# Kernel tuning notes

Measured on AMD Instinct MI355X. Metric: run time of the kernel, lower is better.

Reference implementation:

```python
import jax, jax.numpy as jnp
import numpy as np
from jax import lax

B, N = 8, 4096
NPOINT, RADIUS, NSAMPLE = 1024, 0.2, 32
MLP = [64, 64, 128]
FEAT = 64
ALPHA = 0.2          # LeakyReLU slope
BN_EPS = 1e-5        # BatchNorm eps (eval mode, running_mean=0, running_var=1)
BIG = 1e10


def setup_inputs() -> dict:
    key = jax.random.key(0)
    ks = jax.random.split(key, 16)
    xyz = jax.random.uniform(ks[0], (B, N, 3), dtype=jnp.float32)
    feats = jax.random.normal(ks[1], (B, N, FEAT), dtype=jnp.float32)
    d = {"points": jnp.concatenate([xyz, feats], axis=-1)}
    ch = [FEAT] + MLP
    for i in range(len(MLP)):
        d[f"W{i}"] = jax.random.normal(ks[2 + 3 * i], (ch[i + 1], ch[i]), dtype=jnp.float32) * 0.1
        d[f"b{i}"] = jnp.zeros((ch[i + 1],), jnp.float32)
        d[f"g{i}"] = jnp.ones((ch[i + 1],), jnp.float32)
        d[f"be{i}"] = jnp.zeros((ch[i + 1],), jnp.float32)
    d["a_att"] = jax.random.uniform(ks[12], (3 + MLP[-1], MLP[-1]), jnp.float32, -0.3, 0.3)
    return d


def _gather(points, idx):
    # points: [B, N, D], idx: [B, ...] -> [B, ..., D]
    return jax.vmap(lambda p, i: p[i])(points, idx)


def farthest_point_sample(xyz, npoint):
    # xyz: [B, N, 3] -> [B, npoint] (deterministic start at index 0)
    b, n, _ = xyz.shape
    def step(carry, _):
        distance, farthest = carry
        centered = jnp.take_along_axis(xyz, farthest[:, None, None], axis=1)  # [B,1,3]
        dist = jnp.sum((xyz - centered) ** 2, axis=-1)                        # [B,N]
        distance = jnp.minimum(distance, dist)
        return (distance, jnp.argmax(distance, axis=-1)), farthest
    init = (jnp.full((b, n), BIG, dtype=xyz.dtype), jnp.zeros((b,), dtype=jnp.int32))
    _, idxs = lax.scan(step, init, None, length=npoint)
    return jnp.transpose(idxs)  # [B, npoint]


def query_ball_point(nsample, radius, xyz, centered_xyz):
    # squared distances [B, npoint, N]
    d = (-2.0 * jnp.einsum('bpc,bnc->bpn', centered_xyz, xyz)
         + jnp.sum(centered_xyz ** 2, -1)[..., None]
         + jnp.sum(xyz ** 2, -1)[:, None, :])
    d = jnp.where(d > radius ** 2, BIG, d)
    order = jnp.argsort(d, axis=-1)[..., :nsample]                    # [B,np,ns]
    sv = jnp.take_along_axis(d, order, axis=-1)                       # sorted values
    first = order[..., 0:1]
    return jnp.where(sv == BIG, first, order)


def _mlp(x, params):
    # x: [..., C]; 1x1 conv + BN(eval, mean=0, var=1) + relu per layer
    for (W, b, g, be) in params:
        x = jnp.einsum('...c,oc->...o', x, W) + b
        x = x * (g / jnp.sqrt(1.0 + BN_EPS)) + be
        x = jax.nn.relu(x)
    return x


def reference(points, W0, b0, g0, be0, W1, b1, g1, be1, W2, b2, g2, be2, a_att):
    xyz = points[..., :3]
    feats = points[..., 3:]
    cidx = farthest_point_sample(xyz, NPOINT)          # [B, npoint]
    cxyz = _gather(xyz, cidx)                          # [B, npoint, 3]
    cfeat = _gather(feats, cidx)                       # [B, npoint, D]
    gidx = query_ball_point(NSAMPLE, RADIUS, xyz, cxyz)  # [B, npoint, nsample]
    gxyz = _gather(xyz, gidx)                          # [B, npoint, ns, 3]
    gfeat = _gather(feats, gidx)                       # [B, npoint, ns, D]

    params = [(W0, b0, g0, be0), (W1, b1, g1, be1), (W2, b2, g2, be2)]
    cfeat = _mlp(cfeat, params)                        # [B, npoint, D']
    gfeat = _mlp(gfeat, params)                        # [B, npoint, ns, D']

    cpts = jnp.concatenate([cxyz, cfeat], axis=-1)     # [B, npoint, 3+D']
    gpts = jnp.concatenate([gxyz, gfeat], axis=-1)     # [B, npoint, ns, 3+D']

    delta = gpts - cpts[:, :, None, :]
    att = jax.nn.leaky_relu(jnp.einsum('bpnc,cd->bpnd', delta, a_att), ALPHA)
    att = jax.nn.softmax(att, axis=2)                  # over nsample (eval: no dropout)
    gac = jnp.sum(att * gfeat, axis=2)                 # [B, npoint, D']
    return jnp.concatenate([cxyz, gac], axis=-1)       # [B, npoint, 3+D']
```

## Files before the change

### kernel.cpp

```cpp
#include <hip/hip_runtime.h>
#include <math.h>

#define NBATCH 8
#define NPTS 4096
#define NPOINT 1024
#define NSAMPLE 32
#define PTDIM 67
#define BIGF 1e10f

#define DPP_QUAD_XOR1 0xB1
#define DPP_QUAD_XOR2 0x4E
#define DPP_ROW_HALF_MIRROR 0x141
#define DPP_ROW_MIRROR 0x140
#define DPP_ROW_BCAST15 0x142
#define DPP_ROW_BCAST31 0x143

template <int CTRL>
__device__ inline float dpp_mov_f(float v) {
  int i = __float_as_int(v);
  return __int_as_float(__builtin_amdgcn_update_dpp(i, i, CTRL, 0xf, 0xf, false));
}
template <int CTRL>
__device__ inline unsigned dpp_mov_u(unsigned v) {
  return (unsigned)__builtin_amdgcn_update_dpp((int)v, (int)v, CTRL, 0xf, 0xf, false);
}
template <int CTRL>
__device__ inline void dpp_min2(unsigned& hi, unsigned& lo) {
  unsigned nh = dpp_mov_u<CTRL>(hi);
  unsigned nl = dpp_mov_u<CTRL>(lo);
  bool take = (nh < hi) || (nh == hi && nl < lo);
  hi = take ? nh : hi;
  lo = take ? nl : lo;
}
__device__ inline unsigned fmap(float d) {
  unsigned b = __float_as_uint(d);
  return ((int)b < 0) ? ~b : (b | 0x80000000u);
}
#define FMAP_INF 0xFF800000u

__device__ inline float red32_max(float v) {
  v = fmaxf(v, dpp_mov_f<DPP_QUAD_XOR1>(v));
  v = fmaxf(v, dpp_mov_f<DPP_QUAD_XOR2>(v));
  v = fmaxf(v, dpp_mov_f<DPP_ROW_HALF_MIRROR>(v));
  v = fmaxf(v, dpp_mov_f<DPP_ROW_MIRROR>(v));
  v = fmaxf(v, __shfl_xor(v, 16));
  return v;
}
__device__ inline float red32_sum(float v) {
  v += dpp_mov_f<DPP_QUAD_XOR1>(v);
  v += dpp_mov_f<DPP_QUAD_XOR2>(v);
  v += dpp_mov_f<DPP_ROW_HALF_MIRROR>(v);
  v += dpp_mov_f<DPP_ROW_MIRROR>(v);
  v += __shfl_xor(v, 16);
  return v;
}

struct FpsS {
  unsigned long long slots[2][4];
  int cidxS[NPOINT];
  float4 C[NPTS];
};
struct ProjS {
  float As[131 * 128];
  float w0[64 * 64], w1[64 * 64], w2[128 * 64];
  float bb0[64], ss0[64], ee0[64];
  float bb1[64], ss1[64], ee1[64];
  float bb2[128], ss2[128], ee2[128];
};
#define F1_SMEM (sizeof(ProjS) > sizeof(FpsS) ? sizeof(ProjS) : sizeof(FpsS))

__device__ void fps_body(char* smemRaw, const float* __restrict__ pts,
                         int* __restrict__ cidx, float* __restrict__ X,
                         float* __restrict__ Y, float* __restrict__ Z) {
#pragma clang fp contract(off)
  FpsS* S = (FpsS*)smemRaw;
  const int b = blockIdx.x, tid = threadIdx.x;
  const int w = tid >> 6, lane = tid & 63;
  const float* pb = pts + (size_t)b * NPTS * PTDIM;
  float2 px2[8], py2[8], pz2[8];
  float dl[16];
  #pragma unroll
  for (int k = 0; k < 16; k++) {
    int j = tid + (k << 8);
    const float* pj = pb + (size_t)j * PTDIM;
    float x = pj[0], y = pj[1], z = pj[2];
    if (k & 1) { px2[k >> 1].y = x; py2[k >> 1].y = y; pz2[k >> 1].y = z; }
    else       { px2[k >> 1].x = x; py2[k >> 1].x = y; pz2[k >> 1].x = z; }
    S->C[j] = make_float4(x, y, z, 0.0f);
    X[b * NPTS + j] = x; Y[b * NPTS + j] = y; Z[b * NPTS + j] = z;
    dl[k] = BIGF;
  }
  __syncthreads();
  int f = 0;
  float4 c0 = S->C[0];
  float cx = c0.x, cy = c0.y, cz = c0.z;
  for (int t = 0; t < NPOINT; t++) {
    if (tid == 0) S->cidxS[t] = f;
    float2 c2x = make_float2(cx, cx);
    float2 c2y = make_float2(cy, cy);
    float2 c2z = make_float2(cz, cz);
    #pragma unroll
    for (int m = 0; m < 8; m++) {
      float2 dx = px2[m] - c2x;
      float2 dy = py2[m] - c2y;
      float2 dz = pz2[m] - c2z;
      float2 d = (dx * dx + dy * dy) + dz * dz;
      dl[2 * m]     = fminf(dl[2 * m],     d.x);
      dl[2 * m + 1] = fminf(dl[2 * m + 1], d.y);
    }
    float u0 = fmaxf(dl[0], dl[1]),  u1 = fmaxf(dl[2], dl[3]);
    float u2 = fmaxf(dl[4], dl[5]),  u3 = fmaxf(dl[6], dl[7]);
    float u4 = fmaxf(dl[8], dl[9]),  u5 = fmaxf(dl[10], dl[11]);
    float u6 = fmaxf(dl[12], dl[13]), u7 = fmaxf(dl[14], dl[15]);
    float v0 = fmaxf(u0, u1), v1 = fmaxf(u2, u3);
    float v2 = fmaxf(u4, u5), v3 = fmaxf(u6, u7);
    float bv = fmaxf(fmaxf(v0, v1), fmaxf(v2, v3));
    float m = bv;
    m = fmaxf(m, dpp_mov_f<DPP_QUAD_XOR1>(m));
    m = fmaxf(m, dpp_mov_f<DPP_QUAD_XOR2>(m));
    m = fmaxf(m, dpp_mov_f<DPP_ROW_HALF_MIRROR>(m));
    m = fmaxf(m, dpp_mov_f<DPP_ROW_MIRROR>(m));
    m = fmaxf(m, dpp_mov_f<DPP_ROW_BCAST15>(m));
    m = fmaxf(m, dpp_mov_f<DPP_ROW_BCAST31>(m));
    unsigned wmaxbits = (unsigned)__builtin_amdgcn_readlane(__float_as_int(m), 63);
    unsigned c_[16];
    #pragma unroll
    for (int k = 0; k < 16; k++)
      c_[k] = (__float_as_uint(dl[k]) == wmaxbits) ? (unsigned)(tid + (k << 8)) : 0xFFFFFFFFu;
    unsigned q0 = min(c_[0], c_[1]),  q1 = min(c_[2], c_[3]);
    unsigned q2 = min(c_[4], c_[5]),  q3 = min(c_[6], c_[7]);
    unsigned q4 = min(c_[8], c_[9]),  q5 = min(c_[10], c_[11]);
    unsigned q6 = min(c_[12], c_[13]), q7 = min(c_[14], c_[15]);
    unsigned r0 = min(q0, q1), r1 = min(q2, q3), r2 = min(q4, q5), r3 = min(q6, q7);
    unsigned cand = min(min(r0, r1), min(r2, r3));
    cand = min(cand, dpp_mov_u<DPP_QUAD_XOR1>(cand));
    cand = min(cand, dpp_mov_u<DPP_QUAD_XOR2>(cand));
    cand = min(cand, dpp_mov_u<DPP_ROW_HALF_MIRROR>(cand));
    cand = min(cand, dpp_mov_u<DPP_ROW_MIRROR>(cand));
    cand = min(cand, dpp_mov_u<DPP_ROW_BCAST15>(cand));
    cand = min(cand, dpp_mov_u<DPP_ROW_BCAST31>(cand));
    unsigned jmin = (unsigned)__builtin_amdgcn_readlane((int)cand, 63);
    if (lane == 0)
      S->slots[t & 1][w] = ((unsigned long long)wmaxbits << 32) |
                           (unsigned long long)(NPTS - 1 - jmin);
    __syncthreads();
    unsigned long long s0 = S->slots[t & 1][0], s1 = S->slots[t & 1][1];
    unsigned long long s2 = S->slots[t & 1][2], s3 = S->slots[t & 1][3];
    unsigned long long m0 = s0 > s1 ? s0 : s1;
    unsigned long long m1 = s2 > s3 ? s2 : s3;
    unsigned long long best = m0 > m1 ? m0 : m1;
    f = NPTS - 1 - (int)(best & 0xFFFFFFFFull);
    float4 cc = S->C[f];
    cx = cc.x; cy = cc.y; cz = cc.z;
  }
  __syncthreads();
  for (int i = tid; i < NPOINT; i += 256) cidx[b * NPOINT + i] = S->cidxS[i];
}

__device__ void projmlp_body(char* smemRaw, const float* __restrict__ pts,
    const float* __restrict__ W0, const float* __restrict__ B0, const float* __restrict__ G0, const float* __restrict__ E0,
    const float* __restrict__ W1, const float* __restrict__ B1, const float* __restrict__ G1, const float* __restrict__ E1,
    const float* __restrict__ W2, const float* __restrict__ B2, const float* __restrict__ G2, const float* __restrict__ E2,
    const float* __restrict__ Aatt,
    float* __restrict__ mfeat, float* __restrict__ P) {
  ProjS* S = (ProjS*)smemRaw;
  const float INVS = 0.99999500003750f;
  const int t = threadIdx.x;
  for (int i = t; i < 131 * 128; i += 256) S->As[i] = Aatt[i];
  for (int i = t; i < 4096; i += 256) { S->w0[i] = W0[i]; S->w1[i] = W1[i]; }
  for (int i = t; i < 8192; i += 256) S->w2[i] = W2[i];
  if (t < 64) {
    S->bb0[t] = B0[t]; S->ss0[t] = G0[t] * INVS; S->ee0[t] = E0[t];
    S->bb1[t] = B1[t]; S->ss1[t] = G1[t] * INVS; S->ee1[t] = E1[t];
  }
  if (t < 128) { S->bb2[t] = B2[t]; S->ss2[t] = G2[t] * INVS; S->ee2[t] = E2[t]; }
  __syncthreads();

  const int pb = blockIdx.x - 8;
  for (int rr = 0; rr < 2; rr++) {
    const size_t r = (size_t)pb * 512 + rr * 256 + t;
    const float* xr = pts + r * PTDIM + 3;
    float x[64];
    #pragma unroll
    for (int c = 0; c < 64; c++) x[c] = xr[c];

    float h1[64];
    #pragma unroll
    for (int o = 0; o < 64; o++) {
      float acc = S->bb0[o];
      #pragma unroll
      for (int c = 0; c < 64; c += 4) {
        float4 wv = *(const float4*)&S->w0[o * 64 + c];
        acc = fmaf(wv.x, x[c], acc);
        acc = fmaf(wv.y, x[c + 1], acc);
        acc = fmaf(wv.z, x[c + 2], acc);
        acc = fmaf(wv.w, x[c + 3], acc);
      }
      h1[o] = fmaxf(fmaf(acc, S->ss0[o], S->ee0[o]), 0.0f);
    }
    float h2[64];
    #pragma unroll
    for (int o = 0; o < 64; o++) {
      float acc = S->bb1[o];
      #pragma unroll
      for (int c = 0; c < 64; c += 4) {
        float4 wv = *(const float4*)&S->w1[o * 64 + c];
        acc = fmaf(wv.x, h1[c], acc);
        acc = fmaf(wv.y, h1[c + 1], acc);
        acc = fmaf(wv.z, h1[c + 2], acc);
        acc = fmaf(wv.w, h1[c + 3], acc);
      }
      h2[o] = fmaxf(fmaf(acc, S->ss1[o], S->ee1[o]), 0.0f);
    }
    float h3[128];
    float* orow = mfeat + r * 128;
    #pragma unroll
    for (int o = 0; o < 128; o += 4) {
      float a0 = S->bb2[o], a1 = S->bb2[o + 1], a2 = S->bb2[o + 2], a3 = S->bb2[o + 3];
      #pragma unroll
      for (int c = 0; c < 64; c += 4) {
        float4 wv0 = *(const float4*)&S->w2[(o    ) * 64 + c];
        float4 wv1 = *(const float4*)&S->w2[(o + 1) * 64 + c];
        float4 wv2 = *(const float4*)&S->w2[(o + 2) * 64 + c];
        float4 wv3 = *(const float4*)&S->w2[(o + 3) * 64 + c];
        a0 = fmaf(wv0.x, h2[c], a0); a0 = fmaf(wv0.y, h2[c+1], a0); a0 = fmaf(wv0.z, h2[c+2], a0); a0 = fmaf(wv0.w, h2[c+3], a0);
        a1 = fmaf(wv1.x, h2[c], a1); a1 = fmaf(wv1.y, h2[c+1], a1); a1 = fmaf(wv1.z, h2[c+2], a1); a1 = fmaf(wv1.w, h2[c+3], a1);
        a2 = fmaf(wv2.x, h2[c], a2); a2 = fmaf(wv2.y, h2[c+1], a2); a2 = fmaf(wv2.z, h2[c+2], a2); a2 = fmaf(wv2.w, h2[c+3], a2);
        a3 = fmaf(wv3.x, h2[c], a3); a3 = fmaf(wv3.y, h2[c+1], a3); a3 = fmaf(wv3.z, h2[c+2], a3); a3 = fmaf(wv3.w, h2[c+3], a3);
      }
      float4 ov;
      ov.x = fmaxf(fmaf(a0, S->ss2[o    ], S->ee2[o    ]), 0.0f);
      ov.y = fmaxf(fmaf(a1, S->ss2[o + 1], S->ee2[o + 1]), 0.0f);
      ov.z = fmaxf(fmaf(a2, S->ss2[o + 2], S->ee2[o + 2]), 0.0f);
      ov.w = fmaxf(fmaf(a3, S->ss2[o + 3], S->ee2[o + 3]), 0.0f);
      h3[o] = ov.x; h3[o + 1] = ov.y; h3[o + 2] = ov.z; h3[o + 3] = ov.w;
      *(float4*)(orow + o) = ov;
    }
    const float* pr = pts + r * PTDIM;
    float x0 = pr[0], y0 = pr[1], z0 = pr[2];
    float* prow = P + r * 128;
    for (int grp = 0; grp < 4; grp++) {
      const int g0 = grp * 32;
      float acc[32];
      #pragma unroll
      for (int j = 0; j < 32; j++) {
        float a0 = S->As[0 * 128 + g0 + j];
        float a1 = S->As[1 * 128 + g0 + j];
        float a2 = S->As[2 * 128 + g0 + j];
        acc[j] = fmaf(z0, a2, fmaf(y0, a1, x0 * a0));
      }
      #pragma unroll
      for (int c = 0; c < 128; c++) {
        float s = h3[c];
        const float* arow = &S->As[(3 + c) * 128 + g0];
        #pragma unroll
        for (int j = 0; j < 32; j += 4) {
          float4 a = *(const float4*)&arow[j];
          acc[j]   = fmaf(s, a.x, acc[j]);
          acc[j+1] = fmaf(s, a.y, acc[j+1]);
          acc[j+2] = fmaf(s, a.z, acc[j+2]);
          acc[j+3] = fmaf(s, a.w, acc[j+3]);
        }
      }
      #pragma unroll
      for (int j = 0; j < 32; j += 4)
        *(float4*)(prow + g0 + j) = make_float4(acc[j], acc[j+1], acc[j+2], acc[j+3]);
    }
  }
}

__global__ __launch_bounds__(256) void f1_kernel(const float* __restrict__ pts,
    const float* __restrict__ W0, const float* __restrict__ B0, const float* __restrict__ G0, const float* __restrict__ E0,
    const float* __restrict__ W1, const float* __restrict__ B1, const float* __restrict__ G1, const float* __restrict__ E1,
    const float* __restrict__ W2, const float* __restrict__ B2, const float* __restrict__ G2, const float* __restrict__ E2,
    const float* __restrict__ Aatt,
    float* __restrict__ mfeat, float* __restrict__ P, int* __restrict__ cidx,
    float* __restrict__ X, float* __restrict__ Y, float* __restrict__ Z) {
  __shared__ __align__(16) char smem[F1_SMEM];
  if (blockIdx.x < 8)
    fps_body(smem, pts, cidx, X, Y, Z);
  else
    projmlp_body(smem, pts, W0, B0, G0, E0, W1, B1, G1, E1, W2, B2, G2, E2,
                 Aatt, mfeat, P);
}

__global__ __launch_bounds__(256) void f2_kernel(
    const float* __restrict__ X, const float* __restrict__ Y, const float* __restrict__ Z,
    const int* __restrict__ cidx, int* __restrict__ gidx) {
  __shared__ float dbuf[4][512];
  __shared__ int   ibuf[4][512];
  const int t = threadIdx.x;
  const int w = t >> 6, lane = t & 63;
  const int pc = blockIdx.x * 4 + w;
  const int b = pc >> 10;
  const float* Xb = X + b * NPTS;
  const float* Yb = Y + b * NPTS;
  const float* Zb = Z + b * NPTS;
  const int cI = cidx[pc];
  const float cx = Xb[cI], cy = Yb[cI], cz = Zb[cI];
  const float sc = __fadd_rn(__fadd_rn(__fmul_rn(cx, cx), __fmul_rn(cy, cy)), __fmul_rn(cz, cz));
  const float R2 = 0.04f;
  int cnt = 0;
  for (int rr = 0; rr < 16; rr++) {
    const int base = rr * 256 + lane * 4;
    float4 px4 = *(const float4*)(Xb + base);
    float4 py4 = *(const float4*)(Yb + base);
    float4 pz4 = *(const float4*)(Zb + base);
    #pragma unroll
    for (int e = 0; e < 4; e++) {
      float px = e == 0 ? px4.x : e == 1 ? px4.y : e == 2 ? px4.z : px4.w;
      float py = e == 0 ? py4.x : e == 1 ? py4.y : e == 2 ? py4.z : py4.w;
      float pz = e == 0 ? pz4.x : e == 1 ? pz4.y : e == 2 ? pz4.z : pz4.w;
      float dot = __fadd_rn(__fadd_rn(__fmul_rn(cx, px), __fmul_rn(cy, py)), __fmul_rn(cz, pz));
      float sx  = __fadd_rn(__fadd_rn(__fmul_rn(px, px), __fmul_rn(py, py)), __fmul_rn(pz, pz));
      float d   = __fadd_rn(__fadd_rn(__fmul_rn(-2.0f, dot), sc), sx);
      bool pred = !(d > R2);
      unsigned long long mask = __ballot(pred);
      if (pred) {
        int pos = cnt + (int)__popcll(mask & ((1ull << lane) - 1ull));
        if (pos < 512) { dbuf[w][pos] = d; ibuf[w][pos] = base + e; }
      }
      cnt += (int)__popcll(mask);
    }
  }
  const int K = cnt < 512 ? cnt : 512;
  unsigned long long kk[8];
  #pragma unroll
  for (int k = 0; k < 8; k++) {
    int pos = lane + 64 * k;
    if (pos < K)
      kk[k] = ((unsigned long long)fmap(dbuf[w][pos]) << 32) | (unsigned)ibuf[w][pos];
    else
      kk[k] = ((unsigned long long)FMAP_INF << 32) | 0x7fffffffu;
  }
  int first = 0;
  int* gout = gidx + pc * NSAMPLE;
  for (int it = 0; it < NSAMPLE; it++) {
    unsigned long long best = kk[0];
    #pragma unroll
    for (int k = 1; k < 8; k++) if (kk[k] < best) best = kk[k];
    unsigned hi = (unsigned)(best >> 32), lo = (unsigned)best;
    dpp_min2<DPP_QUAD_XOR1>(hi, lo);
    dpp_min2<DPP_QUAD_XOR2>(hi, lo);
    dpp_min2<DPP_ROW_HALF_MIRROR>(hi, lo);
    dpp_min2<DPP_ROW_MIRROR>(hi, lo);
    dpp_min2<DPP_ROW_BCAST15>(hi, lo);
    dpp_min2<DPP_ROW_BCAST31>(hi, lo);
    unsigned blo = (unsigned)__builtin_amdgcn_readlane((int)lo, 63);
    #pragma unroll
    for (int k = 0; k < 8; k++)
      if ((unsigned)kk[k] == blo)
        kk[k] = (kk[k] & 0xFFFFFFFFull) | ((unsigned long long)FMAP_INF << 32);
    if (it == 0) first = (int)blo;
    if (lane == 0) gout[it] = (it < K) ? (int)blo : first;
  }
}

__global__ __launch_bounds__(256) void attn_kernel(
    const float* __restrict__ X, const float* __restrict__ Y, const float* __restrict__ Z,
    const float* __restrict__ mfeat, const float* __restrict__ P,
    const int* __restrict__ cidx, const int* __restrict__ gidx,
    float* __restrict__ out) {
  __shared__ float pcS[128];
  const int pc = (blockIdx.x & 7) * 1024 + (blockIdx.x >> 3);
  const int b = pc >> 10;
  const int t = threadIdx.x;
  const int n = t & 31, q = t >> 5;
  const int cI = cidx[pc];
  if (t < 128) pcS[t] = P[((size_t)b * NPTS + cI) * 128 + t];
  const int g = gidx[pc * NSAMPLE + n];
  const float* Pg = P + ((size_t)b * NPTS + g) * 128 + q * 16;
  const float* Gf = mfeat + ((size_t)b * NPTS + g) * 128 + q * 16;
  __syncthreads();
  float a[16], gfv[16];
  #pragma unroll
  for (int k = 0; k < 4; k++) {
    float4 vg = *(const float4*)(Pg + 4 * k);
    float4 vc = *(const float4*)&pcS[q * 16 + 4 * k];
    float4 vf = *(const float4*)(Gf + 4 * k);
    a[4*k]   = vg.x - vc.x; a[4*k+1] = vg.y - vc.y;
    a[4*k+2] = vg.z - vc.z; a[4*k+3] = vg.w - vc.w;
    gfv[4*k] = vf.x; gfv[4*k+1] = vf.y; gfv[4*k+2] = vf.z; gfv[4*k+3] = vf.w;
  }
  #pragma unroll
  for (int j = 0; j < 16; j++) a[j] = a[j] >= 0.0f ? a[j] : 0.2f * a[j];
  float e[16], s[16], num[16];
  #pragma unroll
  for (int j = 0; j < 16; j++) {
    float mx = red32_max(a[j]);
    e[j] = expf(a[j] - mx);
  }
  #pragma unroll
  for (int j = 0; j < 16; j++) s[j] = red32_sum(e[j]);
  #pragma unroll
  for (int j = 0; j < 16; j++) num[j] = red32_sum(e[j] * gfv[j]);
  if (n == 0) {
    float* orow = out + (size_t)pc * 131;
    #pragma unroll
    for (int j = 0; j < 16; j++) orow[3 + q * 16 + j] = num[j] / s[j];
    if (q == 0) {
      orow[0] = X[b * NPTS + cI]; orow[1] = Y[b * NPTS + cI]; orow[2] = Z[b * NPTS + cI];
    }
  }
}

extern "C" void kernel_launch(void* const* d_in, const int* in_sizes, int n_in,
                              void* d_out, int out_size, void* d_ws, size_t ws_size,
                              hipStream_t stream) {
  const float* points = (const float*)d_in[0];
  const float* W0 = (const float*)d_in[1];
  const float* B0 = (const float*)d_in[2];
  const float* G0 = (const float*)d_in[3];
  const float* E0 = (const float*)d_in[4];
  const float* W1 = (const float*)d_in[5];
  const float* B1 = (const float*)d_in[6];
  const float* G1 = (const float*)d_in[7];
  const float* E1 = (const float*)d_in[8];
  const float* W2 = (const float*)d_in[9];
  const float* B2 = (const float*)d_in[10];
  const float* G2 = (const float*)d_in[11];
  const float* E2 = (const float*)d_in[12];
  const float* Aatt = (const float*)d_in[13];
  float* out = (float*)d_out;

  float* mfeat = (float*)d_ws;
  float* Pw = mfeat + (size_t)NBATCH * NPTS * 128;
  float* Xw = Pw + (size_t)NBATCH * NPTS * 128;
  float* Yw = Xw + NBATCH * NPTS;
  float* Zw = Yw + NBATCH * NPTS;
  int* cidxw = (int*)(Zw + NBATCH * NPTS);
  int* gidxw = cidxw + NBATCH * NPOINT;

  f1_kernel<<<8 + 64, 256, 0, stream>>>(points,
      W0, B0, G0, E0, W1, B1, G1, E1, W2, B2, G2, E2, Aatt,
      mfeat, Pw, cidxw, Xw, Yw, Zw);
  f2_kernel<<<NBATCH * NPOINT / 4, 256, 0, stream>>>(Xw, Yw, Zw, cidxw, gidxw);
  attn_kernel<<<NBATCH * NPOINT, 256, 0, stream>>>(Xw, Yw, Zw, mfeat, Pw, cidxw, gidxw, out);
}
```

Measured before the change: 833.5 us.

## Fuse ball query with attention and forward FPS winner coordinates through slots

The ball-query kernel and the attention kernel are merged, so each block computes neighbour indices for four centroids into shared memory and then runs the softmax aggregation on them. This removes the gidx round trip through global memory and one kernel launch. In FPS, each wave now writes its candidate's coordinates next to its key in the slot, so the winner's coordinates are picked by selects instead of a dependent shared-memory load after the barrier. The cost is larger shared slots and a serial four-centroid attention loop per block, which lowers the number of parallel blocks in the attention phase.

```diff
diff --git a/kernel.cpp b/kernel.cpp
--- a/kernel.cpp
+++ b/kernel.cpp
@@ -38,6 +38,10 @@
 }
 #define FMAP_INF 0xFF800000u
 
+__device__ inline float4 sel4(bool c, float4 a, float4 b) {
+  return make_float4(c ? a.x : b.x, c ? a.y : b.y, c ? a.z : b.z, c ? a.w : b.w);
+}
+
 __device__ inline float red32_max(float v) {
   v = fmaxf(v, dpp_mov_f<DPP_QUAD_XOR1>(v));
   v = fmaxf(v, dpp_mov_f<DPP_QUAD_XOR2>(v));
@@ -55,8 +59,9 @@
   return v;
 }
 
+struct __align__(16) Slot { float4 c; unsigned long long key; unsigned long long pad; };
 struct FpsS {
-  unsigned long long slots[2][4];
+  Slot slots[2][4];
   int cidxS[NPOINT];
   float4 C[NPTS];
 };
@@ -140,18 +145,21 @@
     cand = min(cand, dpp_mov_u<DPP_ROW_BCAST15>(cand));
     cand = min(cand, dpp_mov_u<DPP_ROW_BCAST31>(cand));
     unsigned jmin = (unsigned)__builtin_amdgcn_readlane((int)cand, 63);
-    if (lane == 0)
-      S->slots[t & 1][w] = ((unsigned long long)wmaxbits << 32) |
-                           (unsigned long long)(NPTS - 1 - jmin);
+    float4 cc = S->C[jmin];
+    unsigned long long key = ((unsigned long long)wmaxbits << 32) |
+                             (unsigned long long)(NPTS - 1 - jmin);
+    const int p = t & 1;
+    if (lane == 0) { S->slots[p][w].c = cc; S->slots[p][w].key = key; }
     __syncthreads();
-    unsigned long long s0 = S->slots[t & 1][0], s1 = S->slots[t & 1][1];
-    unsigned long long s2 = S->slots[t & 1][2], s3 = S->slots[t & 1][3];
-    unsigned long long m0 = s0 > s1 ? s0 : s1;
-    unsigned long long m1 = s2 > s3 ? s2 : s3;
-    unsigned long long best = m0 > m1 ? m0 : m1;
-    f = NPTS - 1 - (int)(best & 0xFFFFFFFFull);
-    float4 cc = S->C[f];
-    cx = cc.x; cy = cc.y; cz = cc.z;
+    unsigned long long k0 = S->slots[p][0].key, k1 = S->slots[p][1].key;
+    unsigned long long k2 = S->slots[p][2].key, k3 = S->slots[p][3].key;
+    float4 cA = S->slots[p][0].c, cB = S->slots[p][1].c;
+    float4 cC = S->slots[p][2].c, cD = S->slots[p][3].c;
+    bool b1 = k1 > k0; unsigned long long ka = b1 ? k1 : k0; float4 ca = sel4(b1, cB, cA);
+    bool b2 = k3 > k2; unsigned long long kb = b2 ? k3 : k2; float4 cb = sel4(b2, cD, cC);
+    bool b3 = kb > ka; unsigned long long kbest = b3 ? kb : ka; float4 cbest = sel4(b3, cb, ca);
+    f = NPTS - 1 - (int)(kbest & 0xFFFFFFFFull);
+    cx = cbest.x; cy = cbest.y; cz = cbest.z;
   }
   __syncthreads();
   for (int i = tid; i < NPOINT; i += 256) cidx[b * NPOINT + i] = S->cidxS[i];
@@ -284,20 +292,33 @@
                  Aatt, mfeat, P);
 }
 
-__global__ __launch_bounds__(256) void f2_kernel(
+__global__ __launch_bounds__(256) void f23_kernel(
     const float* __restrict__ X, const float* __restrict__ Y, const float* __restrict__ Z,
-    const int* __restrict__ cidx, int* __restrict__ gidx) {
+    const int* __restrict__ cidx,
+    const float* __restrict__ mfeat, const float* __restrict__ P,
+    float* __restrict__ out) {
   __shared__ float dbuf[4][512];
   __shared__ int   ibuf[4][512];
+  __shared__ int   gidxS[4][NSAMPLE];
+  __shared__ float pcS[4][128];
+  __shared__ float cxyzS[4][3];
   const int t = threadIdx.x;
   const int w = t >> 6, lane = t & 63;
-  const int pc = blockIdx.x * 4 + w;
-  const int b = pc >> 10;
-  const float* Xb = X + b * NPTS;
-  const float* Yb = Y + b * NPTS;
-  const float* Zb = Z + b * NPTS;
+  const int batch = blockIdx.x & 7;
+  const int grpI = blockIdx.x >> 3;
+  const int pcBase = batch * 1024 + grpI * 4;
+  const int pc = pcBase + w;
+  const float* Xb = X + batch * NPTS;
+  const float* Yb = Y + batch * NPTS;
+  const float* Zb = Z + batch * NPTS;
   const int cI = cidx[pc];
   const float cx = Xb[cI], cy = Yb[cI], cz = Zb[cI];
+  if (lane == 0) { cxyzS[w][0] = cx; cxyzS[w][1] = cy; cxyzS[w][2] = cz; }
+  {
+    const float* pcrow = P + ((size_t)batch * NPTS + cI) * 128;
+    pcS[w][lane] = pcrow[lane];
+    pcS[w][lane + 64] = pcrow[lane + 64];
+  }
   const float sc = __fadd_rn(__fadd_rn(__fmul_rn(cx, cx), __fmul_rn(cy, cy)), __fmul_rn(cz, cz));
   const float R2 = 0.04f;
   int cnt = 0;
@@ -334,7 +355,6 @@
       kk[k] = ((unsigned long long)FMAP_INF << 32) | 0x7fffffffu;
   }
   int first = 0;
-  int* gout = gidx + pc * NSAMPLE;
   for (int it = 0; it < NSAMPLE; it++) {
     unsigned long long best = kk[0];
     #pragma unroll
@@ -352,54 +372,44 @@
       if ((unsigned)kk[k] == blo)
         kk[k] = (kk[k] & 0xFFFFFFFFull) | ((unsigned long long)FMAP_INF << 32);
     if (it == 0) first = (int)blo;
-    if (lane == 0) gout[it] = (it < K) ? (int)blo : first;
-  }
-}
-
-__global__ __launch_bounds__(256) void attn_kernel(
-    const float* __restrict__ X, const float* __restrict__ Y, const float* __restrict__ Z,
-    const float* __restrict__ mfeat, const float* __restrict__ P,
-    const int* __restrict__ cidx, const int* __restrict__ gidx,
-    float* __restrict__ out) {
-  __shared__ float pcS[128];
-  const int pc = (blockIdx.x & 7) * 1024 + (blockIdx.x >> 3);
-  const int b = pc >> 10;
-  const int t = threadIdx.x;
+    if (lane == 0) gidxS[w][it] = (it < K) ? (int)blo : first;
+  }
+  __syncthreads();
   const int n = t & 31, q = t >> 5;
-  const int cI = cidx[pc];
-  if (t < 128) pcS[t] = P[((size_t)b * NPTS + cI) * 128 + t];
-  const int g = gidx[pc * NSAMPLE + n];
-  const float* Pg = P + ((size_t)b * NPTS + g) * 128 + q * 16;
-  const float* Gf = mfeat + ((size_t)b * NPTS + g) * 128 + q * 16;
-  __syncthreads();
-  float a[16], gfv[16];
-  #pragma unroll
-  for (int k = 0; k < 4; k++) {
-    float4 vg = *(const float4*)(Pg + 4 * k);
-    float4 vc = *(const float4*)&pcS[q * 16 + 4 * k];
-    float4 vf = *(const float4*)(Gf + 4 * k);
-    a[4*k]   = vg.x - vc.x; a[4*k+1] = vg.y - vc.y;
-    a[4*k+2] = vg.z - vc.z; a[4*k+3] = vg.w - vc.w;
-    gfv[4*k] = vf.x; gfv[4*k+1] = vf.y; gfv[4*k+2] = vf.z; gfv[4*k+3] = vf.w;
-  }
-  #pragma unroll
-  for (int j = 0; j < 16; j++) a[j] = a[j] >= 0.0f ? a[j] : 0.2f * a[j];
-  float e[16], s[16], num[16];
-  #pragma unroll
-  for (int j = 0; j < 16; j++) {
-    float mx = red32_max(a[j]);
-    e[j] = expf(a[j] - mx);
-  }
-  #pragma unroll
-  for (int j = 0; j < 16; j++) s[j] = red32_sum(e[j]);
-  #pragma unroll
-  for (int j = 0; j < 16; j++) num[j] = red32_sum(e[j] * gfv[j]);
-  if (n == 0) {
-    float* orow = out + (size_t)pc * 131;
-    #pragma unroll
-    for (int j = 0; j < 16; j++) orow[3 + q * 16 + j] = num[j] / s[j];
-    if (q == 0) {
-      orow[0] = X[b * NPTS + cI]; orow[1] = Y[b * NPTS + cI]; orow[2] = Z[b * NPTS + cI];
+  for (int s = 0; s < 4; s++) {
+    const int pcA = pcBase + s;
+    const int g = gidxS[s][n];
+    const float* Pg = P + ((size_t)batch * NPTS + g) * 128 + q * 16;
+    const float* Gf = mfeat + ((size_t)batch * NPTS + g) * 128 + q * 16;
+    float a[16], gfv[16];
+    #pragma unroll
+    for (int k = 0; k < 4; k++) {
+      float4 vg = *(const float4*)(Pg + 4 * k);
+      float4 vc = *(const float4*)&pcS[s][q * 16 + 4 * k];
+      float4 vf = *(const float4*)(Gf + 4 * k);
+      a[4*k]   = vg.x - vc.x; a[4*k+1] = vg.y - vc.y;
+      a[4*k+2] = vg.z - vc.z; a[4*k+3] = vg.w - vc.w;
+      gfv[4*k] = vf.x; gfv[4*k+1] = vf.y; gfv[4*k+2] = vf.z; gfv[4*k+3] = vf.w;
+    }
+    #pragma unroll
+    for (int j = 0; j < 16; j++) a[j] = a[j] >= 0.0f ? a[j] : 0.2f * a[j];
+    float e[16], ssum[16], num[16];
+    #pragma unroll
+    for (int j = 0; j < 16; j++) {
+      float mx = red32_max(a[j]);
+      e[j] = expf(a[j] - mx);
+    }
+    #pragma unroll
+    for (int j = 0; j < 16; j++) ssum[j] = red32_sum(e[j]);
+    #pragma unroll
+    for (int j = 0; j < 16; j++) num[j] = red32_sum(e[j] * gfv[j]);
+    if (n == 0) {
+      float* orow = out + (size_t)pcA * 131;
+      #pragma unroll
+      for (int j = 0; j < 16; j++) orow[3 + q * 16 + j] = num[j] / ssum[j];
+      if (q == 0) {
+        orow[0] = cxyzS[s][0]; orow[1] = cxyzS[s][1]; orow[2] = cxyzS[s][2];
+      }
     }
   }
 }
@@ -429,11 +439,10 @@
   float* Yw = Xw + NBATCH * NPTS;
   float* Zw = Yw + NBATCH * NPTS;
   int* cidxw = (int*)(Zw + NBATCH * NPTS);
-  int* gidxw = cidxw + NBATCH * NPOINT;
 
   f1_kernel<<<8 + 64, 256, 0, stream>>>(points,
       W0, B0, G0, E0, W1, B1, G1, E1, W2, B2, G2, E2, Aatt,
       mfeat, Pw, cidxw, Xw, Yw, Zw);
-  f2_kernel<<<NBATCH * NPOINT / 4, 256, 0, stream>>>(Xw, Yw, Zw, cidxw, gidxw);
-  attn_kernel<<<NBATCH * NPOINT, 256, 0, stream>>>(Xw, Yw, Zw, mfeat, Pw, cidxw, gidxw, out);
-}
+  f23_kernel<<<NBATCH * NPOINT / 4, 256, 0, stream>>>(Xw, Yw, Zw, cidxw,
+                                                      mfeat, Pw, out);
+}
```

After: 854.3 us. +2.5%, slower.
